# Kernel tuning notes

Hardware: AMD Instinct MI355X
Metric: run time of the kernel (lower is better)

The kernel has to match this reference:

```python
import jax, jax.numpy as jnp
import numpy as np

B, S, D, H = 2, 2048, 1024, 16
DK = D // H


def setup_inputs() -> dict:
    key = jax.random.key(0)
    ks = jax.random.split(key, 12)
    scale = 1.0 / np.sqrt(D)
    inp = {
        "pre_Q": jax.random.normal(ks[0], (B, S, D), jnp.float32),
        "pre_K": jax.random.normal(ks[1], (B, S, D), jnp.float32),
        "pre_V": jax.random.normal(ks[2], (B, S, D), jnp.float32),
        "Wq": jax.random.normal(ks[3], (D, D), jnp.float32) * scale,
        "bq": jnp.zeros((D,), jnp.float32),
        "Wk": jax.random.normal(ks[4], (D, D), jnp.float32) * scale,
        "bk": jnp.zeros((D,), jnp.float32),
        "Wv": jax.random.normal(ks[5], (D, D), jnp.float32) * scale,
        "bv": jnp.zeros((D,), jnp.float32),
        "Wo": jax.random.normal(ks[6], (D, D), jnp.float32) * scale,
        "bo": jnp.zeros((D,), jnp.float32),
        "mask": jnp.ones((B, 1, 1, S), jnp.int32),
    }
    return inp


def _split_heads(x):
    # (B, S, D) -> (B, H, S, DK)
    return x.reshape(B, S, H, DK).transpose(0, 2, 1, 3)


def reference(pre_Q, pre_K, pre_V, Wq, bq, Wk, bk, Wv, bv, Wo, bo, mask):
    # linear projections (torch nn.Linear: x @ W.T + b)
    Q = _split_heads(pre_Q @ Wq.T + bq)
    K = _split_heads(pre_K @ Wk.T + bk)
    V = _split_heads(pre_V @ Wv.T + bv)
    # scaled dot-product attention; dropout is identity in eval mode
    scores = jnp.einsum("bhqd,bhkd->bhqk", Q, K) / np.sqrt(DK).astype(np.float32)
    scores = jnp.where(mask == 0, jnp.float32(-1e9), scores)
    weights = jax.nn.softmax(scores, axis=-1)
    ctx = jnp.einsum("bhqk,bhkd->bhqd", weights, V)  # (B, H, S, DK)
    concat = ctx.transpose(0, 2, 1, 3).reshape(B, S, D)
    return concat @ Wo.T + bo
```

## Files before the change

kernel.cpp:

```cpp
#include <hip/hip_runtime.h>

#define SS 2048
#define DD 1024
#define HH 16
#define MM 4096
#define KK 1024

typedef __attribute__((ext_vector_type(8))) short bf16x8;
typedef __attribute__((ext_vector_type(4))) float f32x4;
typedef __attribute__((ext_vector_type(16))) float f32x16;
typedef __attribute__((ext_vector_type(4))) float float4_t;
typedef __attribute__((ext_vector_type(4))) short short4_t;

__device__ __forceinline__ short f2bf(float f) {
    union { float f; unsigned u; } x; x.f = f;
    unsigned r = x.u + 0x7fffu + ((x.u >> 16) & 1u);
    return (short)(r >> 16);
}
__device__ __forceinline__ float bf2f(short s) {
    union { unsigned u; float f; } x; x.u = ((unsigned)(unsigned short)s) << 16;
    return x.f;
}

__device__ __forceinline__ f32x4 mfma16(bf16x8 a, bf16x8 b, f32x4 c) {
    return __builtin_amdgcn_mfma_f32_16x16x32_bf16(a, b, c, 0, 0, 0);
}
__device__ __forceinline__ f32x16 mfma32(bf16x8 a, bf16x8 b, f32x16 c) {
    return __builtin_amdgcn_mfma_f32_32x32x16_bf16(a, b, c, 0, 0, 0);
}

__device__ __forceinline__ void gl_lds16(const void* g, void* l) {
    __builtin_amdgcn_global_load_lds(
        (const __attribute__((address_space(1))) void*)g,
        (__attribute__((address_space(3))) void*)l, 16, 0, 0);
}

__device__ __forceinline__ float exp2a(float x) {
    float r; asm("v_exp_f32 %0, %1" : "=v"(r) : "v"(x)); return r;
}
__device__ __forceinline__ int cvtpk(float lo, float hi) {
    int r; asm("v_cvt_pk_bf16_f32 %0, %1, %2" : "=v"(r) : "v"(lo), "v"(hi)); return r;
}
__device__ __forceinline__ void pswap(int& a, int& b) {
    asm("v_permlane32_swap_b32 %0, %1" : "+v"(a), "+v"(b));
}

__global__ __launch_bounds__(256)
void convX(const float* __restrict__ x0, const float* __restrict__ x1,
           const float* __restrict__ x2, short* __restrict__ dst) {
    const float* s = (blockIdx.y == 0) ? x0 : (blockIdx.y == 1) ? x1 : x2;
    const size_t i = ((size_t)blockIdx.x * 256 + threadIdx.x) * 8;
    float4_t a = *(const float4_t*)(s + i);
    float4_t b = *(const float4_t*)(s + i + 4);
    bf16x8 o;
#pragma unroll
    for (int e = 0; e < 4; ++e) { o[e] = f2bf(a[e]); o[4 + e] = f2bf(b[e]); }
    *(bf16x8*)(dst + (size_t)blockIdx.y * MM * KK + i) = o;
}

__global__ __launch_bounds__(256)
void convW(const float* __restrict__ w0, const float* __restrict__ w1,
           const float* __restrict__ w2, const float* __restrict__ w3,
           short* __restrict__ dst) {
    const float* s = (blockIdx.y == 0) ? w0 : (blockIdx.y == 1) ? w1
                   : (blockIdx.y == 2) ? w2 : w3;
    const size_t i = ((size_t)blockIdx.x * 256 + threadIdx.x) * 8;
    float4_t a = *(const float4_t*)(s + i);
    float4_t b = *(const float4_t*)(s + i + 4);
    bf16x8 o;
#pragma unroll
    for (int e = 0; e < 4; ++e) { o[e] = f2bf(a[e]); o[4 + e] = f2bf(b[e]); }
    *(bf16x8*)(dst + (size_t)blockIdx.y * KK * KK + i) = o;
}

__device__ __forceinline__ void gemm_loop(const short* __restrict__ A,
                                          const short* __restrict__ Bw,
                                          int m0, int n0,
                                          short* As, short* Bs,
                                          f32x4 acc[4][4]) {
    const int tid = threadIdx.x;
    const int lane = tid & 63, w = tid >> 6;
    const int wr = w >> 1, wc = w & 1;
    const int lr = lane & 15, lg = lane >> 4;

    const int r0 = tid >> 3, o0 = (tid & 7) * 8;
    const short* ga = A + (size_t)(m0 + r0) * KK + o0;
    const short* gb = Bw + (size_t)(n0 + r0) * KK + o0;
    char* lA = (char*)As + tid * 16;
    char* lB = (char*)Bs + tid * 16;

#define GSTAGE(buf, kofs)                                                     \
    { _Pragma("unroll")                                                       \
      for (int j = 0; j < 4; ++j) {                                           \
          gl_lds16(ga + (size_t)j * 32 * KK + (kofs), lA + (buf) * 16384 + j * 4096); \
          gl_lds16(gb + (size_t)j * 32 * KK + (kofs), lB + (buf) * 16384 + j * 4096); \
      } }

    GSTAGE(0, 0);
    __syncthreads();
    int cur = 0;
    for (int kt = 0; kt < KK / 64; ++kt) {
        if (kt + 1 < KK / 64) GSTAGE(cur ^ 1, (kt + 1) * 64);
        const char* ba = (const char*)As + cur * 16384;
        const char* bb = (const char*)Bs + cur * 16384;
#pragma unroll
        for (int ks = 0; ks < 2; ++ks) {
            bf16x8 af[4], bfr[4];
#pragma unroll
            for (int i = 0; i < 4; ++i) {
                af[i]  = *(const bf16x8*)(ba + (wr * 64 + i * 16 + lr) * 128 + ks * 64 + lg * 16);
                bfr[i] = *(const bf16x8*)(bb + (wc * 64 + i * 16 + lr) * 128 + ks * 64 + lg * 16);
            }
#pragma unroll
            for (int mi = 0; mi < 4; ++mi)
#pragma unroll
                for (int ni = 0; ni < 4; ++ni)
                    acc[mi][ni] = mfma16(af[mi], bfr[ni], acc[mi][ni]);
        }
        __syncthreads();
        cur ^= 1;
    }
#undef GSTAGE
}

__global__ __launch_bounds__(256, 2)
void qkv_gemm(const short* __restrict__ Xb, const short* __restrict__ Wb,
              const float* __restrict__ bq, const float* __restrict__ bk,
              const float* __restrict__ bv,
              short* __restrict__ Qo, short* __restrict__ Ko, short* __restrict__ Vto) {
    __shared__ __align__(16) short As[2 * 8192];
    __shared__ __align__(16) short Bs[2 * 8192];
    const int z = blockIdx.z;
    const short* A = Xb + (size_t)z * MM * KK;
    const short* W = Wb + (size_t)z * KK * KK;
    const float* bias = (z == 0) ? bq : (z == 1) ? bk : bv;
    const float scale = (z == 0) ? 0.125f * 1.44269504088896f : 1.0f;
    const int m0 = blockIdx.x * 128, n0 = blockIdx.y * 128;

    f32x4 zero = {0.f, 0.f, 0.f, 0.f};
    f32x4 acc[4][4];
#pragma unroll
    for (int i = 0; i < 4; ++i)
#pragma unroll
        for (int j = 0; j < 4; ++j) acc[i][j] = zero;

    gemm_loop(A, W, m0, n0, As, Bs, acc);

    const int tid = threadIdx.x;
    const int lane = tid & 63, w = tid >> 6;
    const int wr = w >> 1, wc = w & 1;
    const int lr = lane & 15, lg = lane >> 4;

#pragma unroll
    for (int mi = 0; mi < 4; ++mi) {
        const int mbase = m0 + wr * 64 + mi * 16 + lg * 4;
        const int b = mbase >> 11, s = mbase & 2047;
#pragma unroll
        for (int ni = 0; ni < 4; ++ni) {
            const int n = n0 + wc * 64 + ni * 16 + lr;
            const float bvv = bias[n];
            const int h = n >> 6, dk = n & 63;
            if (z == 2) {
                short4_t pk;
#pragma unroll
                for (int r = 0; r < 4; ++r) pk[r] = f2bf(acc[mi][ni][r] + bvv);
                *(short4_t*)(Vto + ((size_t)((b * HH + h) * 64 + dk) << 11) + s) = pk;
            } else {
                short* dst = (z == 0) ? Qo : Ko;
#pragma unroll
                for (int r = 0; r < 4; ++r)
                    dst[((size_t)((b * HH + h) * SS + (s + r)) << 6) + dk] =
                        f2bf((acc[mi][ni][r] + bvv) * scale);
            }
        }
    }
}

__global__ __launch_bounds__(256, 2)
void out_gemm(const short* __restrict__ ctx, const short* __restrict__ Wo,
              const float* __restrict__ bo, float* __restrict__ out) {
    __shared__ __align__(16) short As[2 * 8192];
    __shared__ __align__(16) short Bs[2 * 8192];
    const int m0 = blockIdx.x * 128, n0 = blockIdx.y * 128;

    f32x4 zero = {0.f, 0.f, 0.f, 0.f};
    f32x4 acc[4][4];
#pragma unroll
    for (int i = 0; i < 4; ++i)
#pragma unroll
        for (int j = 0; j < 4; ++j) acc[i][j] = zero;

    gemm_loop(ctx, Wo, m0, n0, As, Bs, acc);

    const int tid = threadIdx.x;
    const int lane = tid & 63, w = tid >> 6;
    const int wr = w >> 1, wc = w & 1;
    const int lr = lane & 15, lg = lane >> 4;

#pragma unroll
    for (int mi = 0; mi < 4; ++mi)
#pragma unroll
        for (int ni = 0; ni < 4; ++ni) {
            const int n = n0 + wc * 64 + ni * 16 + lr;
            const float bvv = bo[n];
#pragma unroll
            for (int r = 0; r < 4; ++r) {
                const int m = m0 + wr * 64 + mi * 16 + lg * 4 + r;
                out[(size_t)m * KK + n] = acc[mi][ni][r] + bvv;
            }
        }
}

__global__ __launch_bounds__(256, 4)
void attn_kernel(const short* __restrict__ Qg, const short* __restrict__ Kg,
                 const short* __restrict__ Vtg, const int* __restrict__ mask,
                 short* __restrict__ Po, float* __restrict__ Pm, float* __restrict__ Pl) {
    __shared__ __align__(16) short Ks[2][4096];
    __shared__ __align__(16) short Vs[2][4096];

    const int tid = threadIdx.x, w = tid >> 6, lane = tid & 63;
    const int l31 = lane & 31, hi = lane >> 5;
    const int bh = blockIdx.y, b = bh >> 4;
    const int half = blockIdx.z;
    const int q0w = blockIdx.x * 128 + w * 32;

    const short* Qh = Qg + (size_t)bh * SS * 64;
    const short* Kh = Kg + (size_t)bh * SS * 64;
    const short* Vh = Vtg + (size_t)bh * 64 * SS;
    const int* mrow = mask + b * SS;

    bf16x8 qf[4];
#pragma unroll
    for (int t = 0; t < 4; ++t)
        qf[t] = *(const bf16x8*)(Qh + (q0w + l31) * 64 + t * 16 + hi * 8);

    f32x16 octx0, octx1;
#pragma unroll
    for (int r = 0; r < 16; ++r) { octx0[r] = 0.f; octx1[r] = 0.f; }
    float mrun = -1e30f, lrun = 0.f;

    const int tq = (tid >> 6) & 3;
    const short* gk0 = Kh + (l31) * 64 + tq * 16 + hi * 8;
    const short* gk1 = Kh + (32 + l31) * 64 + tq * 16 + hi * 8;
    const short* gv0 = Vh + (size_t)(l31) * SS + tq * 16 + hi * 8;
    const short* gv1 = Vh + (size_t)(32 + l31) * SS + tq * 16 + hi * 8;
    char* lK = (char*)Ks + tid * 16;
    char* lV = (char*)Vs + tid * 16;

#define ASTAGE(buf, key0)                                      \
    { gl_lds16(gk0 + (key0) * 64, lK + (buf) * 8192);          \
      gl_lds16(gk1 + (key0) * 64, lK + 4096 + (buf) * 8192);   \
      gl_lds16(gv0 + (key0), lV + (buf) * 8192);               \
      gl_lds16(gv1 + (key0), lV + 4096 + (buf) * 8192); }

    const int it0 = half * (SS / 128), it1 = it0 + (SS / 128);
    ASTAGE(0, it0 * 64);
    __syncthreads();
    int cur = 0;

    for (int it = it0; it < it1; ++it) {
        const int key0 = it * 64;
        if (it + 1 < it1) ASTAGE(cur ^ 1, key0 + 64);

        const char* cK = (const char*)Ks + cur * 8192;
        const char* cV = (const char*)Vs + cur * 8192;

        f32x16 s0, s1;
#pragma unroll
        for (int r = 0; r < 16; ++r) { s0[r] = 0.f; s1[r] = 0.f; }
#pragma unroll
        for (int t = 0; t < 4; ++t) {
            bf16x8 a0 = *(const bf16x8*)(cK + ((0 * 4 + t) * 64 + lane) * 16);
            bf16x8 a1 = *(const bf16x8*)(cK + ((1 * 4 + t) * 64 + lane) * 16);
            s0 = mfma32(a0, qf[t], s0);
            s1 = mfma32(a1, qf[t], s1);
        }

        const int mk = mrow[key0 + lane];
        if (!__all(mk != 0)) {
#pragma unroll
            for (int r = 0; r < 16; ++r) {
                const int kl = (r & 3) + 8 * (r >> 2) + 4 * hi;
                if (mrow[key0 + kl] == 0) s0[r] = -1e9f;
                if (mrow[key0 + 32 + kl] == 0) s1[r] = -1e9f;
            }
        }

        float tv[16];
#pragma unroll
        for (int r = 0; r < 16; ++r) tv[r] = fmaxf(s0[r], s1[r]);
#pragma unroll
        for (int off = 8; off >= 1; off >>= 1)
#pragma unroll
            for (int r = 0; r < 8; ++r)
                if (r < off) tv[r] = fmaxf(tv[r], tv[r + off]);
        float tm = tv[0];
        tm = fmaxf(tm, __shfl_xor(tm, 32));

        if (!__all(tm <= mrun + 8.0f)) {
            const float mnew = fmaxf(mrun, tm);
            const float alpha = exp2a(mrun - mnew);
            lrun *= alpha;
#pragma unroll
            for (int r = 0; r < 16; ++r) {
                const int ql = (r & 3) + 8 * (r >> 2) + 4 * hi;
                const float aq = __shfl(alpha, ql);
                octx0[r] *= aq;
                octx1[r] *= aq;
            }
            mrun = mnew;
        }

#pragma unroll
        for (int r = 0; r < 16; ++r) {
            s0[r] = exp2a(s0[r] - mrun);
            s1[r] = exp2a(s1[r] - mrun);
        }
        float sv[16];
#pragma unroll
        for (int r = 0; r < 16; ++r) sv[r] = s0[r] + s1[r];
#pragma unroll
        for (int off = 8; off >= 1; off >>= 1)
#pragma unroll
            for (int r = 0; r < 8; ++r)
                if (r < off) sv[r] += sv[r + off];
        float rs = sv[0];
        rs += __shfl_xor(rs, 32);
        lrun += rs;

        bf16x8 pa[4];
#pragma unroll
        for (int kb = 0; kb < 2; ++kb) {
            const f32x16& sv16 = kb ? s1 : s0;
#pragma unroll
            for (int halfp = 0; halfp < 2; ++halfp) {
                const int base = halfp * 8;
                int A  = cvtpk(sv16[base + 0], sv16[base + 1]);
                int Bw = cvtpk(sv16[base + 2], sv16[base + 3]);
                int Cw = cvtpk(sv16[base + 4], sv16[base + 5]);
                int Dw = cvtpk(sv16[base + 6], sv16[base + 7]);
                pswap(A, Cw);
                pswap(Bw, Dw);
                union { int wv[4]; bf16x8 v; } u;
                u.wv[0] = A; u.wv[1] = Bw; u.wv[2] = Cw; u.wv[3] = Dw;
                pa[kb * 2 + halfp] = u.v;
            }
        }

#pragma unroll
        for (int kk = 0; kk < 4; ++kk) {
            bf16x8 v0 = *(const bf16x8*)(cV + ((0 * 4 + kk) * 64 + lane) * 16);
            bf16x8 v1 = *(const bf16x8*)(cV + ((1 * 4 + kk) * 64 + lane) * 16);
            octx0 = mfma32(pa[kk], v0, octx0);
            octx1 = mfma32(pa[kk], v1, octx1);
        }

        __syncthreads();
        cur ^= 1;
    }
#undef ASTAGE

    const size_t pbase = (size_t)(half * 32 + bh) * SS;
#pragma unroll
    for (int r = 0; r < 16; ++r) {
        const int ql = (r & 3) + 8 * (r >> 2) + 4 * hi;
        short* prow = Po + (pbase + q0w + ql) * 64 + l31;
        prow[0]  = f2bf(octx0[r]);
        prow[32] = f2bf(octx1[r]);
    }
    if (hi == 0) {
        Pm[pbase + q0w + l31] = mrun;
        Pl[pbase + q0w + l31] = lrun;
    }
}

__global__ __launch_bounds__(256)
void attn_combine(const short* __restrict__ Po, const float* __restrict__ Pm,
                  const float* __restrict__ Pl, short* __restrict__ ctxb) {
    const int idx = blockIdx.x * 256 + threadIdx.x;
    const int d0 = (idx & 7) * 8;
    const int s  = (idx >> 3) & (SS - 1);
    const int bh = idx >> 14;
    const int b = bh >> 4, h = bh & 15;

    const size_t i1 = (size_t)bh * SS + s;
    const size_t i2 = (size_t)(32 + bh) * SS + s;
    const float m1 = Pm[i1], m2 = Pm[i2];
    const float l1 = Pl[i1], l2 = Pl[i2];
    const float m = fmaxf(m1, m2);
    const float w1 = exp2a(m1 - m), w2 = exp2a(m2 - m);
    const float inv = 1.f / (l1 * w1 + l2 * w2);

    bf16x8 o1 = *(const bf16x8*)(Po + i1 * 64 + d0);
    bf16x8 o2 = *(const bf16x8*)(Po + i2 * 64 + d0);
    bf16x8 o;
#pragma unroll
    for (int j = 0; j < 8; ++j)
        o[j] = f2bf((bf2f(o1[j]) * w1 + bf2f(o2[j]) * w2) * inv);
    *(bf16x8*)(ctxb + ((size_t)(b * SS + s)) * DD + h * 64 + d0) = o;
}

extern "C" void kernel_launch(void* const* d_in, const int* in_sizes, int n_in,
                              void* d_out, int out_size, void* d_ws, size_t ws_size,
                              hipStream_t stream) {
    const float* preQ = (const float*)d_in[0];
    const float* preK = (const float*)d_in[1];
    const float* preV = (const float*)d_in[2];
    const float* Wq   = (const float*)d_in[3];
    const float* bq   = (const float*)d_in[4];
    const float* Wk   = (const float*)d_in[5];
    const float* bk   = (const float*)d_in[6];
    const float* Wv   = (const float*)d_in[7];
    const float* bv   = (const float*)d_in[8];
    const float* Wo   = (const float*)d_in[9];
    const float* bo   = (const float*)d_in[10];
    const int*   mask = (const int*)d_in[11];
    float* out = (float*)d_out;

    char* ws = (char*)d_ws;
    short* Xb  = (short*)(ws);
    short* Wb  = (short*)(ws + (size_t)25165824);
    short* Qw  = (short*)(ws + (size_t)33554432);
    short* Kw  = (short*)(ws + (size_t)41943040);
    short* Vtw = (short*)(ws + (size_t)50331648);
    short* Ctx = (short*)(ws + (size_t)58720256);
    short* Po  = (short*)(ws + (size_t)67108864);
    float* Pm  = (float*)(ws + (size_t)83886080);
    float* Pl  = (float*)(ws + (size_t)84410368);

    convX<<<dim3(2048, 3), 256, 0, stream>>>(preQ, preK, preV, Xb);
    convW<<<dim3(512, 4), 256, 0, stream>>>(Wq, Wk, Wv, Wo, Wb);
    qkv_gemm<<<dim3(32, 8, 3), 256, 0, stream>>>(Xb, Wb, bq, bk, bv, Qw, Kw, Vtw);
    attn_kernel<<<dim3(16, 32, 2), 256, 0, stream>>>(Qw, Kw, Vtw, mask, Po, Pm, Pl);
    attn_combine<<<dim3(2048), 256, 0, stream>>>(Po, Pm, Pl, Ctx);
    out_gemm<<<dim3(32, 8), 256, 0, stream>>>(Ctx, Wb + (size_t)3 * KK * KK, bo, out);
}
```

Before: 263.4 us.

## Merge conversion kernels, fragment-ordered LDS staging, narrower out-projection tiles

Merges the two fp32-to-bf16 conversion kernels into one launch. Rewrites the GEMM staging so global-to-LDS copies place data in MFMA fragment order, making each lane's LDS reads contiguous and avoiding the strided row accesses that could cause bank conflicts. The GEMM core is templated on N-tile width, and the output projection uses 128x64 tiles to double its block count (256 to 512) for better CU fill. The tradeoff is fewer MFMAs per loaded A tile in the output GEMM.

After: 270.6 us. +2.8%, slower.

```diff
diff --git a/kernel.cpp b/kernel.cpp
--- a/kernel.cpp
+++ b/kernel.cpp
@@ -46,75 +46,97 @@
 }
 
 __global__ __launch_bounds__(256)
-void convX(const float* __restrict__ x0, const float* __restrict__ x1,
-           const float* __restrict__ x2, short* __restrict__ dst) {
-    const float* s = (blockIdx.y == 0) ? x0 : (blockIdx.y == 1) ? x1 : x2;
-    const size_t i = ((size_t)blockIdx.x * 256 + threadIdx.x) * 8;
-    float4_t a = *(const float4_t*)(s + i);
-    float4_t b = *(const float4_t*)(s + i + 4);
+void conv_all(const float* __restrict__ x0, const float* __restrict__ x1,
+              const float* __restrict__ x2,
+              const float* __restrict__ w0, const float* __restrict__ w1,
+              const float* __restrict__ w2, const float* __restrict__ w3,
+              short* __restrict__ Xb, short* __restrict__ Wb) {
+    const int bid = blockIdx.x;
+    const float* src;
+    short* dst;
+    size_t i;
+    if (bid < 6144) {
+        const int plane = bid >> 11, idx = bid & 2047;
+        src = (plane == 0) ? x0 : (plane == 1) ? x1 : x2;
+        i = ((size_t)idx * 256 + threadIdx.x) * 8;
+        dst = Xb + (size_t)plane * MM * KK;
+    } else {
+        const int b2 = bid - 6144;
+        const int plane = b2 >> 9, idx = b2 & 511;
+        src = (plane == 0) ? w0 : (plane == 1) ? w1 : (plane == 2) ? w2 : w3;
+        i = ((size_t)idx * 256 + threadIdx.x) * 8;
+        dst = Wb + (size_t)plane * KK * KK;
+    }
+    float4_t a = *(const float4_t*)(src + i);
+    float4_t b = *(const float4_t*)(src + i + 4);
     bf16x8 o;
 #pragma unroll
     for (int e = 0; e < 4; ++e) { o[e] = f2bf(a[e]); o[4 + e] = f2bf(b[e]); }
-    *(bf16x8*)(dst + (size_t)blockIdx.y * MM * KK + i) = o;
-}
-
-__global__ __launch_bounds__(256)
-void convW(const float* __restrict__ w0, const float* __restrict__ w1,
-           const float* __restrict__ w2, const float* __restrict__ w3,
-           short* __restrict__ dst) {
-    const float* s = (blockIdx.y == 0) ? w0 : (blockIdx.y == 1) ? w1
-                   : (blockIdx.y == 2) ? w2 : w3;
-    const size_t i = ((size_t)blockIdx.x * 256 + threadIdx.x) * 8;
-    float4_t a = *(const float4_t*)(s + i);
-    float4_t b = *(const float4_t*)(s + i + 4);
-    bf16x8 o;
-#pragma unroll
-    for (int e = 0; e < 4; ++e) { o[e] = f2bf(a[e]); o[4 + e] = f2bf(b[e]); }
-    *(bf16x8*)(dst + (size_t)blockIdx.y * KK * KK + i) = o;
-}
-
-__device__ __forceinline__ void gemm_loop(const short* __restrict__ A,
+    *(bf16x8*)(dst + i) = o;
+}
+
+template <int NI>
+__device__ __forceinline__ void gemm_core(const short* __restrict__ A,
                                           const short* __restrict__ Bw,
                                           int m0, int n0,
-                                          short* As, short* Bs,
-                                          f32x4 acc[4][4]) {
+                                          char* As, char* Bs,
+                                          f32x4 acc[4][NI]) {
     const int tid = threadIdx.x;
     const int lane = tid & 63, w = tid >> 6;
     const int wr = w >> 1, wc = w & 1;
-    const int lr = lane & 15, lg = lane >> 4;
-
-    const int r0 = tid >> 3, o0 = (tid & 7) * 8;
-    const short* ga = A + (size_t)(m0 + r0) * KK + o0;
-    const short* gb = Bw + (size_t)(n0 + r0) * KK + o0;
-    char* lA = (char*)As + tid * 16;
-    char* lB = (char*)Bs + tid * 16;
-
-#define GSTAGE(buf, kofs)                                                     \
-    { _Pragma("unroll")                                                       \
-      for (int j = 0; j < 4; ++j) {                                           \
-          gl_lds16(ga + (size_t)j * 32 * KK + (kofs), lA + (buf) * 16384 + j * 4096); \
-          gl_lds16(gb + (size_t)j * 32 * KK + (kofs), lB + (buf) * 16384 + j * 4096); \
-      } }
+
+    const short* srcA[4];
+#pragma unroll
+    for (int jj = 0; jj < 4; ++jj) {
+        const int c = tid + jj * 256;
+        const int arow = ((c >> 9) << 6) + (((c >> 7) & 3) << 4) + (c & 15);
+        const int akc  = (((c >> 6) & 1) << 2) + ((c >> 4) & 3);
+        srcA[jj] = A + (size_t)(m0 + arow) * KK + akc * 8;
+    }
+    const short* srcB[NI];
+#pragma unroll
+    for (int jj = 0; jj < NI; ++jj) {
+        const int c = tid + jj * 256;
+        const int wcb = c / (NI * 128), rem = c % (NI * 128);
+        const int brow = wcb * (16 * NI) + ((rem >> 7) << 4) + (c & 15);
+        const int bkc  = (((c >> 6) & 1) << 2) + ((c >> 4) & 3);
+        srcB[jj] = Bw + (size_t)(n0 + brow) * KK + bkc * 8;
+    }
+    char* ldA = As + tid * 16;
+    char* ldB = Bs + tid * 16;
+    constexpr int ABYTES = 16384;
+    constexpr int BBYTES = NI * 4096;
+
+#define GSTAGE(buf, kofs)                                                   \
+    { _Pragma("unroll")                                                     \
+      for (int jj = 0; jj < 4; ++jj)                                        \
+          gl_lds16(srcA[jj] + (kofs), ldA + (buf) * ABYTES + jj * 4096);    \
+      _Pragma("unroll")                                                     \
+      for (int jj = 0; jj < NI; ++jj)                                       \
+          gl_lds16(srcB[jj] + (kofs), ldB + (buf) * BBYTES + jj * 4096); }
 
     GSTAGE(0, 0);
     __syncthreads();
     int cur = 0;
+    const int Ab = wr * 8192 + lane * 16;
+    const int Bb = wc * (NI * 2048) + lane * 16;
     for (int kt = 0; kt < KK / 64; ++kt) {
         if (kt + 1 < KK / 64) GSTAGE(cur ^ 1, (kt + 1) * 64);
-        const char* ba = (const char*)As + cur * 16384;
-        const char* bb = (const char*)Bs + cur * 16384;
+        const char* ba = As + cur * ABYTES + Ab;
+        const char* bb = Bs + cur * BBYTES + Bb;
 #pragma unroll
         for (int ks = 0; ks < 2; ++ks) {
-            bf16x8 af[4], bfr[4];
-#pragma unroll
-            for (int i = 0; i < 4; ++i) {
-                af[i]  = *(const bf16x8*)(ba + (wr * 64 + i * 16 + lr) * 128 + ks * 64 + lg * 16);
-                bfr[i] = *(const bf16x8*)(bb + (wc * 64 + i * 16 + lr) * 128 + ks * 64 + lg * 16);
-            }
+            bf16x8 af[4], bfr[NI];
+#pragma unroll
+            for (int i = 0; i < 4; ++i)
+                af[i] = *(const bf16x8*)(ba + i * 2048 + ks * 1024);
+#pragma unroll
+            for (int ni = 0; ni < NI; ++ni)
+                bfr[ni] = *(const bf16x8*)(bb + ni * 2048 + ks * 1024);
 #pragma unroll
             for (int mi = 0; mi < 4; ++mi)
 #pragma unroll
-                for (int ni = 0; ni < 4; ++ni)
+                for (int ni = 0; ni < NI; ++ni)
                     acc[mi][ni] = mfma16(af[mi], bfr[ni], acc[mi][ni]);
         }
         __syncthreads();
@@ -128,8 +150,8 @@
               const float* __restrict__ bq, const float* __restrict__ bk,
               const float* __restrict__ bv,
               short* __restrict__ Qo, short* __restrict__ Ko, short* __restrict__ Vto) {
-    __shared__ __align__(16) short As[2 * 8192];
-    __shared__ __align__(16) short Bs[2 * 8192];
+    __shared__ __align__(16) char As[2 * 16384];
+    __shared__ __align__(16) char Bs[2 * 16384];
     const int z = blockIdx.z;
     const short* A = Xb + (size_t)z * MM * KK;
     const short* W = Wb + (size_t)z * KK * KK;
@@ -144,7 +166,7 @@
 #pragma unroll
         for (int j = 0; j < 4; ++j) acc[i][j] = zero;
 
-    gemm_loop(A, W, m0, n0, As, Bs, acc);
+    gemm_core<4>(A, W, m0, n0, As, Bs, acc);
 
     const int tid = threadIdx.x;
     const int lane = tid & 63, w = tid >> 6;
@@ -179,18 +201,18 @@
 __global__ __launch_bounds__(256, 2)
 void out_gemm(const short* __restrict__ ctx, const short* __restrict__ Wo,
               const float* __restrict__ bo, float* __restrict__ out) {
-    __shared__ __align__(16) short As[2 * 8192];
-    __shared__ __align__(16) short Bs[2 * 8192];
-    const int m0 = blockIdx.x * 128, n0 = blockIdx.y * 128;
+    __shared__ __align__(16) char As[2 * 16384];
+    __shared__ __align__(16) char Bs[2 * 8192];
+    const int m0 = blockIdx.x * 128, n0 = blockIdx.y * 64;
 
     f32x4 zero = {0.f, 0.f, 0.f, 0.f};
-    f32x4 acc[4][4];
+    f32x4 acc[4][2];
 #pragma unroll
     for (int i = 0; i < 4; ++i)
 #pragma unroll
-        for (int j = 0; j < 4; ++j) acc[i][j] = zero;
-
-    gemm_loop(ctx, Wo, m0, n0, As, Bs, acc);
+        for (int j = 0; j < 2; ++j) acc[i][j] = zero;
+
+    gemm_core<2>(ctx, Wo, m0, n0, As, Bs, acc);
 
     const int tid = threadIdx.x;
     const int lane = tid & 63, w = tid >> 6;
@@ -200,8 +222,8 @@
 #pragma unroll
     for (int mi = 0; mi < 4; ++mi)
 #pragma unroll
-        for (int ni = 0; ni < 4; ++ni) {
-            const int n = n0 + wc * 64 + ni * 16 + lr;
+        for (int ni = 0; ni < 2; ++ni) {
+            const int n = n0 + wc * 32 + ni * 16 + lr;
             const float bvv = bo[n];
 #pragma unroll
             for (int r = 0; r < 4; ++r) {
@@ -428,10 +450,9 @@
     float* Pm  = (float*)(ws + (size_t)83886080);
     float* Pl  = (float*)(ws + (size_t)84410368);
 
-    convX<<<dim3(2048, 3), 256, 0, stream>>>(preQ, preK, preV, Xb);
-    convW<<<dim3(512, 4), 256, 0, stream>>>(Wq, Wk, Wv, Wo, Wb);
+    conv_all<<<dim3(8192), 256, 0, stream>>>(preQ, preK, preV, Wq, Wk, Wv, Wo, Xb, Wb);
     qkv_gemm<<<dim3(32, 8, 3), 256, 0, stream>>>(Xb, Wb, bq, bk, bv, Qw, Kw, Vtw);
     attn_kernel<<<dim3(16, 32, 2), 256, 0, stream>>>(Qw, Kw, Vtw, mask, Po, Pm, Pl);
     attn_combine<<<dim3(2048), 256, 0, stream>>>(Po, Pm, Pl, Ctx);
-    out_gemm<<<dim3(32, 8), 256, 0, stream>>>(Ctx, Wb + (size_t)3 * KK * KK, bo, out);
-}
+    out_gemm<<<dim3(32, 16), 256, 0, stream>>>(Ctx, Wb + (size_t)3 * KK * KK, bo, out);
+}
```
